# Kernel tuning notes

Hardware: AMD Instinct MI355X
Metric: run time of the kernel (lower is better)

## Reference

```python
import jax, jax.numpy as jnp
import numpy as np

N = 20000
E = 320000
D = 256
OUT = 256
NEG_SLOPE = 0.2


def setup_inputs() -> dict:
    key = jax.random.key(0)
    ks = jax.random.split(key, 16)
    s = 1.0 / np.sqrt(D)
    x = jax.random.normal(ks[0], (N, D), dtype=jnp.float32)
    edge_index = jax.random.randint(ks[1], (2, E), 0, N, dtype=jnp.int64)
    W1 = jax.random.uniform(ks[2], (D, D), jnp.float32, -s, s)
    W2 = jax.random.uniform(ks[3], (D, D), jnp.float32, -s, s)
    Ws = jax.random.uniform(ks[4], (6, D, D), jnp.float32, -s, s)      # per-layer GATConv lin weight
    a_src = jax.random.uniform(ks[5], (6, D), jnp.float32, -s, s)      # per-layer att_src
    a_dst = jax.random.uniform(ks[6], (6, D), jnp.float32, -s, s)      # per-layer att_dst
    bias = jnp.zeros((6, D), dtype=jnp.float32)                        # per-layer GATConv bias
    W3 = jax.random.uniform(ks[7], (2 * D, OUT), jnp.float32, -s, s)
    return {"x": x, "edge_index": edge_index, "W1": W1, "W2": W2,
            "Ws": Ws, "a_src": a_src, "a_dst": a_dst, "bias": bias, "W3": W3}


def _gat_layer(h, src, dst, W, asrc, adst, b):
    # h: [N, D] -> linear transform
    hw = h @ W                                         # [N, D]
    e_src = hw @ asrc                                  # [N]
    e_dst = hw @ adst                                  # [N]
    e = jax.nn.leaky_relu(e_src[src] + e_dst[dst], NEG_SLOPE)  # [E]
    # softmax over incoming edges per destination node
    m = jax.ops.segment_max(e, dst, num_segments=N)    # [N], -inf for empty segs (unused)
    ee = jnp.exp(e - m[dst])                           # [E]
    denom = jax.ops.segment_sum(ee, dst, num_segments=N)
    alpha = ee / denom[dst]                            # [E]
    msg = alpha[:, None] * hw[src]                     # [E, D]
    out = jax.ops.segment_sum(msg, dst, num_segments=N)  # [N, D]
    return out + b


def reference(x, edge_index, W1, W2, Ws, a_src, a_dst, bias, W3):
    src, dst = edge_index[0], edge_index[1]
    h = x @ W1
    h = h @ W2
    for i in range(6):
        h = _gat_layer(h, src, dst, Ws[i], a_src[i], a_dst[i], bias[i])
    h = jnp.concatenate((h, h), axis=1)   # [N, 2D]
    h = jax.nn.relu(h)
    return h @ W3                          # [N, OUT]
```

## Files before the change

### kernel.cpp

```cpp
#include <hip/hip_runtime.h>
#include <hip/hip_fp16.h>
#include <stdint.h>

#define NNODES 20000
#define EEDGES 320000
#define DD     256
#define NEG_SLOPE 0.2f
#define SCAN_BLOCKS ((NNODES + 255) / 256)

typedef _Float16 half8 __attribute__((ext_vector_type(8)));
typedef _Float16 half4 __attribute__((ext_vector_type(4)));
typedef float f32x4 __attribute__((ext_vector_type(4)));


__global__ void zero_ints_k(int* __restrict__ p, int n) {
    int i = blockIdx.x * 256 + threadIdx.x;
    if (i < n) p[i] = 0;
}

__global__ void hist_k(const int* __restrict__ dst, int* __restrict__ rowptr) {
    int i = blockIdx.x * 256 + threadIdx.x;
    if (i < EEDGES) atomicAdd(&rowptr[dst[i] + 1], 1);
}

__global__ __launch_bounds__(256) void scan1_k(int* __restrict__ rowptr, int* __restrict__ bsums) {
    __shared__ int buf[256];
    int idx = blockIdx.x * 256 + threadIdx.x;
    int v = (idx < NNODES) ? rowptr[idx + 1] : 0;
    buf[threadIdx.x] = v;
    __syncthreads();
#pragma unroll
    for (int off = 1; off < 256; off <<= 1) {
        int t = (threadIdx.x >= (unsigned)off) ? buf[threadIdx.x - off] : 0;
        __syncthreads();
        buf[threadIdx.x] += t;
        __syncthreads();
    }
    if (idx < NNODES) rowptr[idx + 1] = buf[threadIdx.x];
    if (threadIdx.x == 255) bsums[blockIdx.x] = buf[255];
}

__global__ __launch_bounds__(128) void scan2_k(int* __restrict__ bsums) {
    __shared__ int buf[128];
    int v = (threadIdx.x < SCAN_BLOCKS) ? bsums[threadIdx.x] : 0;
    buf[threadIdx.x] = v;
    __syncthreads();
#pragma unroll
    for (int off = 1; off < 128; off <<= 1) {
        int t = (threadIdx.x >= (unsigned)off) ? buf[threadIdx.x - off] : 0;
        __syncthreads();
        buf[threadIdx.x] += t;
        __syncthreads();
    }
    if (threadIdx.x < SCAN_BLOCKS) bsums[threadIdx.x] = buf[threadIdx.x];
}

__global__ void scan3_k(int* __restrict__ rowptr, const int* __restrict__ bsums,
                        int* __restrict__ cursor) {
    int idx = blockIdx.x * 256 + threadIdx.x;
    if (idx < NNODES) {
        int v = rowptr[idx + 1];
        if (blockIdx.x > 0) { v += bsums[blockIdx.x - 1]; rowptr[idx + 1] = v; }
        if (idx + 1 < NNODES) cursor[idx + 1] = v;
        if (idx == 0) cursor[0] = 0;
    }
}

__global__ void scatter_k(const int* __restrict__ src, const int* __restrict__ dst,
                          int* __restrict__ cursor, int* __restrict__ colsrc) {
    int i = blockIdx.x * 256 + threadIdx.x;
    if (i < EEDGES) {
        int d = dst[i];
        int pos = atomicAdd(&cursor[d], 1);
        colsrc[pos] = src[i];
    }
}


__global__ void cvt_split_k(const float* __restrict__ X, _Float16* __restrict__ Xh,
                            _Float16* __restrict__ Xl, int n) {
    int i = blockIdx.x * 256 + threadIdx.x;
    if (i < n) {
        float v = X[i];
        _Float16 hi = (_Float16)v;
        Xh[i] = hi;
        Xl[i] = (_Float16)(v - (float)hi);
    }
}


template<bool SUM>
__global__ void cvt_w_k(const float* __restrict__ W, _Float16* __restrict__ Wh,
                        _Float16* __restrict__ Wl) {
    int i = blockIdx.x * 256 + threadIdx.x;
    if (i < DD * DD) {
        int k = i >> 8, n = i & 255;
        float v = W[i];
        if (SUM) v += W[i + DD * DD];
        _Float16 hi = (_Float16)v;
        Wh[n * DD + k] = hi;
        Wl[n * DD + k] = (_Float16)(v - (float)hi);
    }
}


template<bool OUT_SPLIT>
__global__ __launch_bounds__(512, 4) void gemm_k(
    const _Float16* __restrict__ Ah, const _Float16* __restrict__ Al,
    const _Float16* __restrict__ Bh, const _Float16* __restrict__ Bl,
    float* __restrict__ C, _Float16* __restrict__ Ch, _Float16* __restrict__ Cl, int M)
{
    __shared__ _Float16 smem[24576];
    _Float16* sAh = smem;
    _Float16* sAl = smem + 4096;
    _Float16* sBh = smem + 8192;
    _Float16* sBl = smem + 16384;

    const int t = threadIdx.x;
    const int lane = t & 63;
    const int w = t >> 6;
    const int rowBase = blockIdx.y * 64;
    const int colBase = blockIdx.x * 128;
    const int mo = (w & 1) * 32;
    const int no = (w >> 1) * 32;

    const int arow = t >> 3;
    const int slot = t & 7;
    const int swz = (slot ^ (arow & 7)) << 3;

    f32x4 acc[2][2];
#pragma unroll
    for (int m = 0; m < 2; ++m)
#pragma unroll
        for (int n = 0; n < 2; ++n) acc[m][n] = (f32x4){0.f, 0.f, 0.f, 0.f};

    int4 pa_h, pa_l, pb_h0, pb_h1, pb_l0, pb_l1;

#define LOADSTAGE(S) { \
        size_t aoff  = (size_t)(rowBase + arow) * DD + (S) * 64 + slot * 8; \
        size_t boff0 = (size_t)(colBase + arow) * DD + (S) * 64 + slot * 8; \
        size_t boff1 = boff0 + (size_t)64 * DD; \
        pa_h  = *(const int4*)(Ah + aoff); \
        pa_l  = *(const int4*)(Al + aoff); \
        pb_h0 = *(const int4*)(Bh + boff0); \
        pb_h1 = *(const int4*)(Bh + boff1); \
        pb_l0 = *(const int4*)(Bl + boff0); \
        pb_l1 = *(const int4*)(Bl + boff1); \
    }

#define WRITESTAGE() { \
        int da  = arow * 64 + swz; \
        *(int4*)(sAh + da) = pa_h; \
        *(int4*)(sAl + da) = pa_l; \
        *(int4*)(sBh + da) = pb_h0; \
        *(int4*)(sBh + da + 4096) = pb_h1; \
        *(int4*)(sBl + da) = pb_l0; \
        *(int4*)(sBl + da + 4096) = pb_l1; \
    }

    LOADSTAGE(0);
    const int fr = lane & 15;
    const int fq = lane >> 4;

    for (int s = 0; s < 4; ++s) {
        __syncthreads();
        WRITESTAGE();
        __syncthreads();
        if (s < 3) { LOADSTAGE(s + 1); }

#pragma unroll
        for (int kk = 0; kk < 2; ++kk) {
            const int c = kk * 4 + fq;
            half8 ah[2], al[2], bh[2], bl[2];
#pragma unroll
            for (int m = 0; m < 2; ++m) {
                int ra = mo + m * 16 + fr;
                int oa = ra * 64 + ((c ^ (ra & 7)) << 3);
                ah[m] = *(const half8*)(sAh + oa);
                al[m] = *(const half8*)(sAl + oa);
            }
#pragma unroll
            for (int n = 0; n < 2; ++n) {
                int rb = no + n * 16 + fr;
                int ob = rb * 64 + ((c ^ (rb & 7)) << 3);
                bh[n] = *(const half8*)(sBh + ob);
                bl[n] = *(const half8*)(sBl + ob);
            }
#pragma unroll
            for (int m = 0; m < 2; ++m)
#pragma unroll
                for (int n = 0; n < 2; ++n) {
                    acc[m][n] = __builtin_amdgcn_mfma_f32_16x16x32_f16(ah[m], bh[n], acc[m][n], 0, 0, 0);
                    acc[m][n] = __builtin_amdgcn_mfma_f32_16x16x32_f16(ah[m], bl[n], acc[m][n], 0, 0, 0);
                    acc[m][n] = __builtin_amdgcn_mfma_f32_16x16x32_f16(al[m], bh[n], acc[m][n], 0, 0, 0);
                    acc[m][n] = __builtin_amdgcn_mfma_f32_16x16x32_f16(al[m], bl[n], acc[m][n], 0, 0, 0);
                }
        }
    }
#undef LOADSTAGE
#undef WRITESTAGE

    const int ccol = lane & 15;
    const int crq = (lane >> 4) * 4;

    if (OUT_SPLIT) {
        __syncthreads();
#pragma unroll
        for (int m = 0; m < 2; ++m)
#pragma unroll
            for (int n = 0; n < 2; ++n)
#pragma unroll
                for (int r = 0; r < 4; ++r) {
                    int row = mo + m * 16 + crq + r;
                    int col = no + n * 16 + ccol;
                    float v = acc[m][n][r];
                    _Float16 hi = (_Float16)v;
                    smem[row * 136 + col] = hi;
                    smem[8704 + row * 136 + col] = (_Float16)(v - (float)hi);
                }
        __syncthreads();
#pragma unroll
        for (int i = 0; i < 2; ++i) {
            int slotId = i * 512 + t;
            int srow = slotId >> 4;
            int sc = slotId & 15;
            int grow = rowBase + srow;
            if (grow < M) {
                half8 hv = *(const half8*)(smem + srow * 136 + sc * 8);
                half8 lv = *(const half8*)(smem + 8704 + srow * 136 + sc * 8);
                *(half8*)(Ch + (size_t)grow * DD + colBase + sc * 8) = hv;
                *(half8*)(Cl + (size_t)grow * DD + colBase + sc * 8) = lv;
            }
        }
    } else {
#pragma unroll
        for (int m = 0; m < 2; ++m) {
            int growb = rowBase + mo + m * 16 + crq;
#pragma unroll
            for (int n = 0; n < 2; ++n) {
                int gcol = colBase + no + n * 16 + ccol;
#pragma unroll
                for (int r = 0; r < 4; ++r) {
                    int grow = growb + r;
                    if (grow < M) C[(size_t)grow * DD + gcol] = acc[m][n][r];
                }
            }
        }
    }
}


__global__ __launch_bounds__(256) void dots_k(const float* __restrict__ hw,
                                              const float* __restrict__ asrc,
                                              const float* __restrict__ adst,
                                              float* __restrict__ es, float* __restrict__ ed) {
    int wave = threadIdx.x >> 6;
    int lane = threadIdx.x & 63;
    int node = blockIdx.x * 4 + wave;
    if (node >= NNODES) return;
    float4 v = *(const float4*)(hw + (size_t)node * DD + lane * 4);
    float4 a = *(const float4*)(asrc + lane * 4);
    float4 b = *(const float4*)(adst + lane * 4);
    float s = v.x * a.x + v.y * a.y + v.z * a.z + v.w * a.w;
    float d = v.x * b.x + v.y * b.y + v.z * b.z + v.w * b.w;
#pragma unroll
    for (int off = 32; off; off >>= 1) {
        s += __shfl_xor(s, off);
        d += __shfl_xor(d, off);
    }
    if (lane == 0) { es[node] = s; ed[node] = d; }
}


template<bool RELU>
__global__ __launch_bounds__(256, 4) void gat_agg_k(const float* __restrict__ hw,
                                                    const float* __restrict__ es,
                                                    const float* __restrict__ ed,
                                                    const int* __restrict__ rowptr,
                                                    const int* __restrict__ colsrc,
                                                    float* __restrict__ ealpha,
                                                    const float* __restrict__ bias,
                                                    _Float16* __restrict__ hh,
                                                    _Float16* __restrict__ hl) {
    int wave = threadIdx.x >> 6;
    int lane = threadIdx.x & 63;
    int node = blockIdx.x * 4 + wave;
    if (node >= NNODES) return;
    int start = rowptr[node], end = rowptr[node + 1];
    int deg = end - start;
    float edd = ed[node];

    float4 acc0 = make_float4(0.f, 0.f, 0.f, 0.f);
    float4 acc1 = acc0, acc2 = acc0, acc3 = acc0;

#define FMA4(ACC, W_, V) \
    ACC.x = fmaf(W_, V.x, ACC.x); ACC.y = fmaf(W_, V.y, ACC.y); \
    ACC.z = fmaf(W_, V.z, ACC.z); ACC.w = fmaf(W_, V.w, ACC.w);

    if (deg > 0 && deg <= 64) {
        bool valid = lane < deg;
        int msrc = valid ? colsrc[start + lane] : 0;
        float e = valid ? es[msrc] + edd : -INFINITY;
        e = fmaxf(e, NEG_SLOPE * e);
        float mx = e;
#pragma unroll
        for (int off = 32; off; off >>= 1) mx = fmaxf(mx, __shfl_xor(mx, off));
        float ee = valid ? expf(e - mx) : 0.f;
        float sum = ee;
#pragma unroll
        for (int off = 32; off; off >>= 1) sum += __shfl_xor(sum, off);
        float w = ee / sum;

#define FETCH8(V, W_, JB) \
        _Pragma("unroll") \
        for (int q = 0; q < 8; ++q) { \
            int sq = __shfl(msrc, (JB) + q); \
            W_[q] = __shfl(w, (JB) + q); \
            V[q] = *(const float4*)(hw + (size_t)sq * DD + lane * 4); \
        }

#define FMA8(V, W_) \
        FMA4(acc0, W_[0], V[0]); FMA4(acc1, W_[1], V[1]); \
        FMA4(acc2, W_[2], V[2]); FMA4(acc3, W_[3], V[3]); \
        FMA4(acc0, W_[4], V[4]); FMA4(acc1, W_[5], V[5]); \
        FMA4(acc2, W_[6], V[6]); FMA4(acc3, W_[7], V[7]);

        float4 va[8], vb[8];
        float wa[8], wb[8];
        FETCH8(va, wa, 0);
        int jb = 8;
        for (;;) {
            if (jb >= deg) { FMA8(va, wa); break; }
            FETCH8(vb, wb, jb); jb += 8;
            __builtin_amdgcn_sched_barrier(0);
            FMA8(va, wa);
            if (jb >= deg) { FMA8(vb, wb); break; }
            FETCH8(va, wa, jb); jb += 8;
            __builtin_amdgcn_sched_barrier(0);
            FMA8(vb, wb);
        }
#undef FETCH8
#undef FMA8
    } else if (deg > 64) {
        float mx = -INFINITY;
        for (int j = start + lane; j < end; j += 64) {
            float e = es[colsrc[j]] + edd;
            e = fmaxf(e, NEG_SLOPE * e);
            mx = fmaxf(mx, e);
        }
#pragma unroll
        for (int off = 32; off; off >>= 1) mx = fmaxf(mx, __shfl_xor(mx, off));
        float sum = 0.f;
        for (int j = start + lane; j < end; j += 64) {
            float e = es[colsrc[j]] + edd;
            e = fmaxf(e, NEG_SLOPE * e);
            float ee = expf(e - mx);
            ealpha[j] = ee;
            sum += ee;
        }
#pragma unroll
        for (int off = 32; off; off >>= 1) sum += __shfl_xor(sum, off);
        float inv = 1.f / sum;
        int j = start;
        for (; j + 4 <= end; j += 4) {
            int s0 = colsrc[j], s1 = colsrc[j + 1], s2 = colsrc[j + 2], s3 = colsrc[j + 3];
            float w0 = ealpha[j] * inv, w1 = ealpha[j + 1] * inv;
            float w2 = ealpha[j + 2] * inv, w3 = ealpha[j + 3] * inv;
            float4 v0 = *(const float4*)(hw + (size_t)s0 * DD + lane * 4);
            float4 v1 = *(const float4*)(hw + (size_t)s1 * DD + lane * 4);
            float4 v2 = *(const float4*)(hw + (size_t)s2 * DD + lane * 4);
            float4 v3 = *(const float4*)(hw + (size_t)s3 * DD + lane * 4);
            FMA4(acc0, w0, v0); FMA4(acc1, w1, v1);
            FMA4(acc2, w2, v2); FMA4(acc3, w3, v3);
        }
        for (; j < end; ++j) {
            int s0 = colsrc[j];
            float w0 = ealpha[j] * inv;
            float4 v0 = *(const float4*)(hw + (size_t)s0 * DD + lane * 4);
            FMA4(acc0, w0, v0);
        }
    }
#undef FMA4

    acc0.x += acc1.x; acc0.y += acc1.y; acc0.z += acc1.z; acc0.w += acc1.w;
    acc2.x += acc3.x; acc2.y += acc3.y; acc2.z += acc3.z; acc2.w += acc3.w;
    acc0.x += acc2.x; acc0.y += acc2.y; acc0.z += acc2.z; acc0.w += acc2.w;
    float4 b4 = *(const float4*)(bias + lane * 4);
    acc0.x += b4.x; acc0.y += b4.y; acc0.z += b4.z; acc0.w += b4.w;
    if (RELU) {
        acc0.x = fmaxf(acc0.x, 0.f); acc0.y = fmaxf(acc0.y, 0.f);
        acc0.z = fmaxf(acc0.z, 0.f); acc0.w = fmaxf(acc0.w, 0.f);
    }
    size_t base = (size_t)node * DD + lane * 4;
    _Float16 h0 = (_Float16)acc0.x, h1 = (_Float16)acc0.y;
    _Float16 h2 = (_Float16)acc0.z, h3 = (_Float16)acc0.w;
    half4 hv; hv[0] = h0; hv[1] = h1; hv[2] = h2; hv[3] = h3;
    half4 lv;
    lv[0] = (_Float16)(acc0.x - (float)h0); lv[1] = (_Float16)(acc0.y - (float)h1);
    lv[2] = (_Float16)(acc0.z - (float)h2); lv[3] = (_Float16)(acc0.w - (float)h3);
    *(half4*)(hh + base) = hv;
    *(half4*)(hl + base) = lv;
}


extern "C" void kernel_launch(void* const* d_in, const int* in_sizes, int n_in,
                              void* d_out, int out_size, void* d_ws, size_t ws_size,
                              hipStream_t stream) {
    const float* x     = (const float*)d_in[0];
    const int*   ei    = (const int*)d_in[1];
    const float* W1    = (const float*)d_in[2];
    const float* W2    = (const float*)d_in[3];
    const float* Ws    = (const float*)d_in[4];
    const float* a_src = (const float*)d_in[5];
    const float* a_dst = (const float*)d_in[6];
    const float* bias  = (const float*)d_in[7];
    const float* W3    = (const float*)d_in[8];
    float* out = (float*)d_out;

    const int* src = ei;
    const int* dst = ei + EEDGES;

    const size_t ND = (size_t)NNODES * DD;

    float* bufA   = (float*)d_ws;
    float* es     = bufA + ND;
    float* edv    = es + NNODES;
    float* ealpha = edv + NNODES;
    int*   rowptr = (int*)(ealpha + EEDGES);
    int*   cursor = rowptr + (NNODES + 1);
    int*   colsrc = cursor + NNODES;
    int*   bsums  = colsrc + EEDGES;
    _Float16* P0h = (_Float16*)(((uintptr_t)(bsums + SCAN_BLOCKS) + 15) & ~(uintptr_t)15);
    _Float16* P0l = P0h + ND;
    _Float16* P1h = P0l + ND;
    _Float16* P1l = P1h + ND;
    _Float16* WT  = P1l + ND;
    const size_t WSZ = (size_t)DD * DD;

    zero_ints_k<<<(NNODES + 1 + 255) / 256, 256, 0, stream>>>(rowptr, NNODES + 1);
    hist_k<<<(EEDGES + 255) / 256, 256, 0, stream>>>(dst, rowptr);
    scan1_k<<<SCAN_BLOCKS, 256, 0, stream>>>(rowptr, bsums);
    scan2_k<<<1, 128, 0, stream>>>(bsums);
    scan3_k<<<SCAN_BLOCKS, 256, 0, stream>>>(rowptr, bsums, cursor);
    scatter_k<<<(EEDGES + 255) / 256, 256, 0, stream>>>(src, dst, cursor, colsrc);

    const int WBLK = (DD * DD + 255) / 256;
    cvt_w_k<false><<<WBLK, 256, 0, stream>>>(W1, WT + 0 * 2 * WSZ, WT + 0 * 2 * WSZ + WSZ);
    cvt_w_k<false><<<WBLK, 256, 0, stream>>>(W2, WT + 1 * 2 * WSZ, WT + 1 * 2 * WSZ + WSZ);
    for (int l = 0; l < 6; ++l)
        cvt_w_k<false><<<WBLK, 256, 0, stream>>>(Ws + (size_t)l * WSZ,
                                                 WT + (2 + l) * 2 * WSZ,
                                                 WT + (2 + l) * 2 * WSZ + WSZ);
    cvt_w_k<true><<<WBLK, 256, 0, stream>>>(W3, WT + 8 * 2 * WSZ, WT + 8 * 2 * WSZ + WSZ);

    cvt_split_k<<<(int)((ND + 255) / 256), 256, 0, stream>>>(x, P0h, P0l, (int)ND);

    dim3 gg(DD / 128, (NNODES + 63) / 64);
    const int nodeBlocks = (NNODES + 3) / 4;

#define WTH(i) (WT + (i) * 2 * WSZ)
#define WTL(i) (WT + (i) * 2 * WSZ + WSZ)

    gemm_k<true><<<gg, 512, 0, stream>>>(P0h, P0l, WTH(0), WTL(0), nullptr, P1h, P1l, NNODES);
    gemm_k<true><<<gg, 512, 0, stream>>>(P1h, P1l, WTH(1), WTL(1), nullptr, P0h, P0l, NNODES);

    for (int l = 0; l < 6; ++l) {
        gemm_k<false><<<gg, 512, 0, stream>>>(P0h, P0l, WTH(2 + l), WTL(2 + l),
                                              bufA, nullptr, nullptr, NNODES);
        dots_k<<<nodeBlocks, 256, 0, stream>>>(bufA, a_src + (size_t)l * DD,
                                               a_dst + (size_t)l * DD, es, edv);
        if (l < 5)
            gat_agg_k<false><<<nodeBlocks, 256, 0, stream>>>(bufA, es, edv, rowptr, colsrc,
                                                             ealpha, bias + (size_t)l * DD,
                                                             P0h, P0l);
        else
            gat_agg_k<true><<<nodeBlocks, 256, 0, stream>>>(bufA, es, edv, rowptr, colsrc,
                                                            ealpha, bias + (size_t)l * DD,
                                                            P0h, P0l);
    }

    gemm_k<false><<<gg, 512, 0, stream>>>(P0h, P0l, WTH(8), WTL(8), out,
                                          nullptr, nullptr, NNODES);
#undef WTH
#undef WTL
}
```

Baseline: 678.7 us.

## Fuse attention dot products into GEMM epilogue and tighten aggregation tail loop

Removes the separate dots_k kernel by computing per-row att_src/att_dst partial dot products inside the GEMM epilogue. Each column block writes its partial sums to a strided buffer, and the aggregation kernel adds the two partials. The aggregation inner loop now handles full groups of 8 neighbors, then a group of 4, then single neighbors, so it no longer runs over padded lanes. It also drops the occupancy hint on gat_agg_k. This saves one kernel launch and one full read of hw per layer, at the cost of extra shared-memory reductions and syncs in the GEMM and one extra gather per edge.

Measured after the change: 641.3 us. -5.5%, faster.

```diff
diff --git a/kernel.cpp b/kernel.cpp
--- a/kernel.cpp
+++ b/kernel.cpp
@@ -7,6 +7,7 @@
 #define DD     256
 #define NEG_SLOPE 0.2f
 #define SCAN_BLOCKS ((NNODES + 255) / 256)
+#define ESTR   20480
 
 typedef _Float16 half8 __attribute__((ext_vector_type(8)));
 typedef _Float16 half4 __attribute__((ext_vector_type(4)));
@@ -104,11 +105,13 @@
 }
 
 
-template<bool OUT_SPLIT>
+template<bool OUT_SPLIT, bool DOTS>
 __global__ __launch_bounds__(512, 4) void gemm_k(
     const _Float16* __restrict__ Ah, const _Float16* __restrict__ Al,
     const _Float16* __restrict__ Bh, const _Float16* __restrict__ Bl,
-    float* __restrict__ C, _Float16* __restrict__ Ch, _Float16* __restrict__ Cl, int M)
+    float* __restrict__ C, _Float16* __restrict__ Ch, _Float16* __restrict__ Cl,
+    const float* __restrict__ asrc, const float* __restrict__ adst,
+    float* __restrict__ esp, float* __restrict__ edp, int M)
 {
     __shared__ _Float16 smem[24576];
     _Float16* sAh = smem;
@@ -203,7 +206,7 @@
     const int ccol = lane & 15;
     const int crq = (lane >> 4) * 4;
 
-    if (OUT_SPLIT) {
+    if constexpr (OUT_SPLIT) {
         __syncthreads();
 #pragma unroll
         for (int m = 0; m < 2; ++m)
@@ -247,48 +250,66 @@
             }
         }
     }
-}
-
-
-__global__ __launch_bounds__(256) void dots_k(const float* __restrict__ hw,
-                                              const float* __restrict__ asrc,
-                                              const float* __restrict__ adst,
-                                              float* __restrict__ es, float* __restrict__ ed) {
-    int wave = threadIdx.x >> 6;
-    int lane = threadIdx.x & 63;
-    int node = blockIdx.x * 4 + wave;
-    if (node >= NNODES) return;
-    float4 v = *(const float4*)(hw + (size_t)node * DD + lane * 4);
-    float4 a = *(const float4*)(asrc + lane * 4);
-    float4 b = *(const float4*)(adst + lane * 4);
-    float s = v.x * a.x + v.y * a.y + v.z * a.z + v.w * a.w;
-    float d = v.x * b.x + v.y * b.y + v.z * b.z + v.w * b.w;
-#pragma unroll
-    for (int off = 32; off; off >>= 1) {
-        s += __shfl_xor(s, off);
-        d += __shfl_xor(d, off);
-    }
-    if (lane == 0) { es[node] = s; ed[node] = d; }
+
+    if constexpr (DOTS) {
+        float as0 = asrc[colBase + no + ccol];
+        float as1 = asrc[colBase + no + 16 + ccol];
+        float ad0 = adst[colBase + no + ccol];
+        float ad1 = adst[colBase + no + 16 + ccol];
+        __syncthreads();
+        float* sred = (float*)smem;
+        const int cw = w >> 1;
+#pragma unroll
+        for (int m = 0; m < 2; ++m)
+#pragma unroll
+            for (int r = 0; r < 4; ++r) {
+                float ps = acc[m][0][r] * as0 + acc[m][1][r] * as1;
+                float pd = acc[m][0][r] * ad0 + acc[m][1][r] * ad1;
+#pragma unroll
+                for (int off = 1; off < 16; off <<= 1) {
+                    ps += __shfl_xor(ps, off);
+                    pd += __shfl_xor(pd, off);
+                }
+                if (ccol == 0) {
+                    int row = mo + m * 16 + crq + r;
+                    sred[row * 8 + cw] = ps;
+                    sred[512 + row * 8 + cw] = pd;
+                }
+            }
+        __syncthreads();
+        if (t < 64) {
+            float esb = sred[t * 8 + 0] + sred[t * 8 + 1] + sred[t * 8 + 2] + sred[t * 8 + 3];
+            float edb = sred[512 + t * 8 + 0] + sred[512 + t * 8 + 1]
+                      + sred[512 + t * 8 + 2] + sred[512 + t * 8 + 3];
+            int grow = rowBase + t;
+            if (grow < M) {
+                esp[(size_t)blockIdx.x * ESTR + grow] = esb;
+                edp[(size_t)blockIdx.x * ESTR + grow] = edb;
+            }
+        }
+    }
 }
 
 
 template<bool RELU>
-__global__ __launch_bounds__(256, 4) void gat_agg_k(const float* __restrict__ hw,
-                                                    const float* __restrict__ es,
-                                                    const float* __restrict__ ed,
-                                                    const int* __restrict__ rowptr,
-                                                    const int* __restrict__ colsrc,
-                                                    float* __restrict__ ealpha,
-                                                    const float* __restrict__ bias,
-                                                    _Float16* __restrict__ hh,
-                                                    _Float16* __restrict__ hl) {
+__global__ __launch_bounds__(256) void gat_agg_k(const float* __restrict__ hw,
+                                                 const float* __restrict__ es0,
+                                                 const float* __restrict__ es1,
+                                                 const float* __restrict__ ed0,
+                                                 const float* __restrict__ ed1,
+                                                 const int* __restrict__ rowptr,
+                                                 const int* __restrict__ colsrc,
+                                                 float* __restrict__ ealpha,
+                                                 const float* __restrict__ bias,
+                                                 _Float16* __restrict__ hh,
+                                                 _Float16* __restrict__ hl) {
     int wave = threadIdx.x >> 6;
     int lane = threadIdx.x & 63;
     int node = blockIdx.x * 4 + wave;
     if (node >= NNODES) return;
     int start = rowptr[node], end = rowptr[node + 1];
     int deg = end - start;
-    float edd = ed[node];
+    float edd = ed0[node] + ed1[node];
 
     float4 acc0 = make_float4(0.f, 0.f, 0.f, 0.f);
     float4 acc1 = acc0, acc2 = acc0, acc3 = acc0;
@@ -300,7 +321,7 @@
     if (deg > 0 && deg <= 64) {
         bool valid = lane < deg;
         int msrc = valid ? colsrc[start + lane] : 0;
-        float e = valid ? es[msrc] + edd : -INFINITY;
+        float e = valid ? es0[msrc] + es1[msrc] + edd : -INFINITY;
         e = fmaxf(e, NEG_SLOPE * e);
         float mx = e;
 #pragma unroll
@@ -325,26 +346,50 @@
         FMA4(acc0, W_[4], V[4]); FMA4(acc1, W_[5], V[5]); \
         FMA4(acc2, W_[6], V[6]); FMA4(acc3, W_[7], V[7]);
 
-        float4 va[8], vb[8];
-        float wa[8], wb[8];
-        FETCH8(va, wa, 0);
-        int jb = 8;
-        for (;;) {
-            if (jb >= deg) { FMA8(va, wa); break; }
-            FETCH8(vb, wb, jb); jb += 8;
-            __builtin_amdgcn_sched_barrier(0);
-            FMA8(va, wa);
-            if (jb >= deg) { FMA8(vb, wb); break; }
-            FETCH8(va, wa, jb); jb += 8;
-            __builtin_amdgcn_sched_barrier(0);
-            FMA8(vb, wb);
+        const int nfull = deg & ~7;
+        if (nfull > 0) {
+            float4 va[8], vb[8];
+            float wa[8], wb[8];
+            FETCH8(va, wa, 0);
+            int jb = 8;
+            for (;;) {
+                if (jb >= nfull) { FMA8(va, wa); break; }
+                FETCH8(vb, wb, jb); jb += 8;
+                __builtin_amdgcn_sched_barrier(0);
+                FMA8(va, wa);
+                if (jb >= nfull) { FMA8(vb, wb); break; }
+                FETCH8(va, wa, jb); jb += 8;
+                __builtin_amdgcn_sched_barrier(0);
+                FMA8(vb, wb);
+            }
+        }
+        int j2 = nfull;
+        if (j2 + 4 <= deg) {
+            int s0 = __shfl(msrc, j2 + 0), s1 = __shfl(msrc, j2 + 1);
+            int s2 = __shfl(msrc, j2 + 2), s3 = __shfl(msrc, j2 + 3);
+            float w0 = __shfl(w, j2 + 0), w1 = __shfl(w, j2 + 1);
+            float w2 = __shfl(w, j2 + 2), w3 = __shfl(w, j2 + 3);
+            float4 v0 = *(const float4*)(hw + (size_t)s0 * DD + lane * 4);
+            float4 v1 = *(const float4*)(hw + (size_t)s1 * DD + lane * 4);
+            float4 v2 = *(const float4*)(hw + (size_t)s2 * DD + lane * 4);
+            float4 v3 = *(const float4*)(hw + (size_t)s3 * DD + lane * 4);
+            FMA4(acc0, w0, v0); FMA4(acc1, w1, v1);
+            FMA4(acc2, w2, v2); FMA4(acc3, w3, v3);
+            j2 += 4;
+        }
+        for (; j2 < deg; ++j2) {
+            int   s0 = __shfl(msrc, j2);
+            float w0 = __shfl(w, j2);
+            float4 v0 = *(const float4*)(hw + (size_t)s0 * DD + lane * 4);
+            FMA4(acc0, w0, v0);
         }
 #undef FETCH8
 #undef FMA8
     } else if (deg > 64) {
         float mx = -INFINITY;
         for (int j = start + lane; j < end; j += 64) {
-            float e = es[colsrc[j]] + edd;
+            int s = colsrc[j];
+            float e = es0[s] + es1[s] + edd;
             e = fmaxf(e, NEG_SLOPE * e);
             mx = fmaxf(mx, e);
         }
@@ -352,7 +397,8 @@
         for (int off = 32; off; off >>= 1) mx = fmaxf(mx, __shfl_xor(mx, off));
         float sum = 0.f;
         for (int j = start + lane; j < end; j += 64) {
-            float e = es[colsrc[j]] + edd;
+            int s = colsrc[j];
+            float e = es0[s] + es1[s] + edd;
             e = fmaxf(e, NEG_SLOPE * e);
             float ee = expf(e - mx);
             ealpha[j] = ee;
@@ -423,9 +469,9 @@
     const size_t ND = (size_t)NNODES * DD;
 
     float* bufA   = (float*)d_ws;
-    float* es     = bufA + ND;
-    float* edv    = es + NNODES;
-    float* ealpha = edv + NNODES;
+    float* es01   = bufA + ND;
+    float* ed01   = es01 + 2 * ESTR;
+    float* ealpha = ed01 + 2 * ESTR;
     int*   rowptr = (int*)(ealpha + EEDGES);
     int*   cursor = rowptr + (NNODES + 1);
     int*   colsrc = cursor + NNODES;
@@ -461,26 +507,31 @@
 #define WTH(i) (WT + (i) * 2 * WSZ)
 #define WTL(i) (WT + (i) * 2 * WSZ + WSZ)
 
-    gemm_k<true><<<gg, 512, 0, stream>>>(P0h, P0l, WTH(0), WTL(0), nullptr, P1h, P1l, NNODES);
-    gemm_k<true><<<gg, 512, 0, stream>>>(P1h, P1l, WTH(1), WTL(1), nullptr, P0h, P0l, NNODES);
+    gemm_k<true, false><<<gg, 512, 0, stream>>>(P0h, P0l, WTH(0), WTL(0), nullptr, P1h, P1l,
+                                                nullptr, nullptr, nullptr, nullptr, NNODES);
+    gemm_k<true, false><<<gg, 512, 0, stream>>>(P1h, P1l, WTH(1), WTL(1), nullptr, P0h, P0l,
+                                                nullptr, nullptr, nullptr, nullptr, NNODES);
 
     for (int l = 0; l < 6; ++l) {
-        gemm_k<false><<<gg, 512, 0, stream>>>(P0h, P0l, WTH(2 + l), WTL(2 + l),
-                                              bufA, nullptr, nullptr, NNODES);
-        dots_k<<<nodeBlocks, 256, 0, stream>>>(bufA, a_src + (size_t)l * DD,
-                                               a_dst + (size_t)l * DD, es, edv);
+        gemm_k<false, true><<<gg, 512, 0, stream>>>(P0h, P0l, WTH(2 + l), WTL(2 + l),
+                                                    bufA, nullptr, nullptr,
+                                                    a_src + (size_t)l * DD, a_dst + (size_t)l * DD,
+                                                    es01, ed01, NNODES);
         if (l < 5)
-            gat_agg_k<false><<<nodeBlocks, 256, 0, stream>>>(bufA, es, edv, rowptr, colsrc,
-                                                             ealpha, bias + (size_t)l * DD,
-                                                             P0h, P0l);
+            gat_agg_k<false><<<nodeBlocks, 256, 0, stream>>>(bufA, es01, es01 + ESTR,
+                                                             ed01, ed01 + ESTR,
+                                                             rowptr, colsrc, ealpha,
+                                                             bias + (size_t)l * DD, P0h, P0l);
         else
-            gat_agg_k<true><<<nodeBlocks, 256, 0, stream>>>(bufA, es, edv, rowptr, colsrc,
-                                                            ealpha, bias + (size_t)l * DD,
-                                                            P0h, P0l);
-    }
-
-    gemm_k<false><<<gg, 512, 0, stream>>>(P0h, P0l, WTH(8), WTL(8), out,
-                                          nullptr, nullptr, NNODES);
+            gat_agg_k<true><<<nodeBlocks, 256, 0, stream>>>(bufA, es01, es01 + ESTR,
+                                                            ed01, ed01 + ESTR,
+                                                            rowptr, colsrc, ealpha,
+                                                            bias + (size_t)l * DD, P0h, P0l);
+    }
+
+    gemm_k<false, false><<<gg, 512, 0, stream>>>(P0h, P0l, WTH(8), WTL(8), out,
+                                                 nullptr, nullptr,
+                                                 nullptr, nullptr, nullptr, nullptr, NNODES);
 #undef WTH
 #undef WTL
 }
```
